# Performance work log

Measured on AMD Instinct MI355X. Metric: run time of the kernel, lower is better.

The kernel has to match this reference:

```python
import jax, jax.numpy as jnp
import numpy as np

WINDOW = 16  # window_size from init_kwargs


def sigmoid_cutoff(x):
    # max(min(1.2*sigmoid(x) - 0.1, 1), 0)
    return jnp.clip(1.2 * jax.nn.sigmoid(x) - 0.1, 0.0, 1.0)


def setup_inputs() -> dict:
    key = jax.random.key(0)
    k1, k2, k3 = jax.random.split(key, 3)
    B, S, H = 8, 2048, 1024
    x = jax.random.normal(k1, (B, S, H), dtype=jnp.float32)
    # Dense kernels (glorot-ish scale), x_layer has no bias, y_layer has bias
    Wx = jax.random.normal(k2, (H, H), dtype=jnp.float32) * (1.0 / np.sqrt(H))
    Wy = jax.random.normal(k3, (H, 2 * H), dtype=jnp.float32) * (1.0 / np.sqrt(H))
    by = jnp.zeros((2 * H,), dtype=jnp.float32)
    return {"x": x, "Wx": Wx, "Wy": Wy, "by": by}


def reference(x, Wx, Wy, by):
    B, S, H = x.shape
    # left-pad sequence with window_size-1 zeros, then project once (x_layer)
    xp = jnp.pad(x, ((0, 0), (WINDOW - 1, 0), (0, 0)))
    proj = jnp.einsum('bsh,hd->bsd', xp, Wx)  # [B, S+W-1, H]

    def step(state, i):
        # inputs[:, i:S+i] in the original loop
        inp = jax.lax.dynamic_slice_in_dim(proj, i, S, axis=1)  # [B,S,H]
        ns = jnp.einsum('bsh,hd->bsd', state, Wy) + by          # [B,S,2H]
        # reshape [B,S,2,H]: channel 0 = candidate, channel 1 = gate
        cand, gate_logits = jnp.split(ns, 2, axis=-1)
        gate = sigmoid_cutoff(gate_logits)
        new_state = jax.nn.relu(gate * (inp + cand) + (1.0 - gate) * state)
        return new_state, None

    state0 = jnp.zeros_like(x)
    state, _ = jax.lax.scan(step, state0, jnp.arange(WINDOW))
    return state
```

## Files before the change

### kernel.cpp

```cpp
#include <hip/hip_runtime.h>

#define H 1024
#define SEQ 2048
#define MROWS 16384
#define KD 1024
#define NT32 32
#define EPW 72

typedef _Float16 f16;
typedef _Float16 f16x8 __attribute__((ext_vector_type(8)));
typedef float f32x4 __attribute__((ext_vector_type(4)));

__device__ __forceinline__ float gate_fn(float x) {
    float s = 1.0f / (1.0f + __expf(-x));
    return fminf(fmaxf(1.2f * s - 0.1f, 0.0f), 1.0f);
}

__device__ __forceinline__ size_t frag_off(int row, int k) {
    return ((size_t)((row >> 4) * 32 + (k >> 5))) * 512
         + (size_t)((((row & 15) | (((k >> 3) & 3) << 4)) << 3) + (k & 7));
}

__device__ __forceinline__ void gload_lds16(const void* g, void* lds) {
    __builtin_amdgcn_global_load_lds(
        (const __attribute__((address_space(1))) unsigned int*)g,
        (__attribute__((address_space(3))) unsigned int*)lds, 16, 0, 0);
}

__global__ void k_f32_to_f16(const float* __restrict__ in, f16* __restrict__ out) {
    size_t i = ((size_t)blockIdx.x * blockDim.x + threadIdx.x) * 8;
    float4 v0 = *(const float4*)(in + i);
    float4 v1 = *(const float4*)(in + i + 4);
    f16x8 o;
    o[0] = (f16)v0.x; o[1] = (f16)v0.y; o[2] = (f16)v0.z; o[3] = (f16)v0.w;
    o[4] = (f16)v1.x; o[5] = (f16)v1.y; o[6] = (f16)v1.z; o[7] = (f16)v1.w;
    *(f16x8*)(out + i) = o;
}

__global__ void k_transpose_f16(const float* __restrict__ Wsrc, f16* __restrict__ WT,
                                int K, int N) {
    __shared__ float tile[32][33];
    int n0 = blockIdx.x * 32, k0 = blockIdx.y * 32;
    for (int i = threadIdx.y; i < 32; i += 8)
        tile[i][threadIdx.x] = Wsrc[(size_t)(k0 + i) * N + n0 + threadIdx.x];
    __syncthreads();
    for (int i = threadIdx.y; i < 32; i += 8)
        WT[(size_t)(n0 + i) * K + k0 + threadIdx.x] = (f16)tile[threadIdx.x][i];
}

__global__ __launch_bounds__(256) void k_proj_gemm(const f16* __restrict__ A,
                                                   const f16* __restrict__ BT,
                                                   f16* __restrict__ P16) {
    __shared__ alignas(16) f16 Alds[128 * 32];
    __shared__ alignas(16) f16 Blds[128 * 32];
    const int tid = threadIdx.x;
    const int lane = tid & 63, wid = tid >> 6;
    const int l15 = lane & 15, l4 = lane >> 4;
    const int bm = blockIdx.x, bn = blockIdx.y;

    const f16* gA[2]; const f16* gB[2];
    char* ldsA[2]; char* ldsB[2];
#pragma unroll
    for (int it = 0; it < 2; ++it) {
        int c = it * 4 + wid;
        int row = c * 16 + (lane >> 2);
        int kch = (lane & 3) ^ ((row >> 1) & 3);
        gA[it] = A + (size_t)(bm * 128 + row) * KD + kch * 8;
        gB[it] = BT + (size_t)(bn * 128 + row) * KD + kch * 8;
        ldsA[it] = (char*)Alds + c * 1024;
        ldsB[it] = (char*)Blds + c * 1024;
    }

    int offA[2], offB[8];
#pragma unroll
    for (int m = 0; m < 2; ++m) {
        int row = wid * 32 + m * 16 + l15;
        offA[m] = row * 64 + ((l4 ^ ((row >> 1) & 3)) << 4);
    }
#pragma unroll
    for (int n = 0; n < 8; ++n) {
        int row = n * 16 + l15;
        offB[n] = row * 64 + ((l4 ^ ((row >> 1) & 3)) << 4);
    }

    f32x4 acc[2][8] = {};

    for (int kt = 0; kt < KD / 32; ++kt) {
        __syncthreads();
#pragma unroll
        for (int it = 0; it < 2; ++it) {
            gload_lds16(gA[it], ldsA[it]);
            gload_lds16(gB[it], ldsB[it]);
            gA[it] += 32; gB[it] += 32;
        }
        __syncthreads();
        f16x8 a[2], b[8];
#pragma unroll
        for (int m = 0; m < 2; ++m) a[m] = *(const f16x8*)((const char*)Alds + offA[m]);
#pragma unroll
        for (int n = 0; n < 8; ++n) b[n] = *(const f16x8*)((const char*)Blds + offB[n]);
#pragma unroll
        for (int n = 0; n < 8; ++n)
#pragma unroll
            for (int m = 0; m < 2; ++m)
                acc[m][n] = __builtin_amdgcn_mfma_f32_16x16x32_f16(a[m], b[n], acc[m][n], 0, 0, 0);
    }

#pragma unroll
    for (int m = 0; m < 2; ++m)
#pragma unroll
        for (int n = 0; n < 8; ++n) {
            int col = bn * 128 + n * 16 + l15;
#pragma unroll
            for (int r = 0; r < 4; ++r) {
                int row = bm * 128 + wid * 32 + m * 16 + l4 * 4 + r;
                P16[(size_t)row * H + col] = (f16)acc[m][n][r];
            }
        }
}

__global__ void k_step0(const f16* __restrict__ P16, const float* __restrict__ by,
                        f16* __restrict__ S16) {
    size_t idx = ((size_t)blockIdx.x * blockDim.x + threadIdx.x) * 8;
    int row = (int)(idx >> 10);
    int d = (int)(idx & 1023);
    int s = row & (SEQ - 1);
    f16x8 p = {};
    if (s >= 15) p = *(const f16x8*)(P16 + (size_t)(row - 15) * H + d);
    float4 byc0 = *(const float4*)(by + d);
    float4 byc1 = *(const float4*)(by + d + 4);
    float4 byg0 = *(const float4*)(by + H + d);
    float4 byg1 = *(const float4*)(by + H + d + 4);
    f16x8 sv;
#pragma unroll
    for (int j = 0; j < 8; ++j) {
        float byc = (j < 4) ? ((const float*)&byc0)[j] : ((const float*)&byc1)[j - 4];
        float byg = (j < 4) ? ((const float*)&byg0)[j] : ((const float*)&byg1)[j - 4];
        float g = gate_fn(byg);
        float v = fmaxf(g * ((float)p[j] + byc), 0.f);
        sv[j] = (f16)v;
    }
    *(f16x8*)(S16 + frag_off(row, d)) = sv;
}

__global__ __launch_bounds__(512, 4) void k_step_gemm(const f16* __restrict__ A,
                                                      const f16* __restrict__ BT,
                                                      const f16* __restrict__ P16,
                                                      const float* __restrict__ by,
                                                      float* __restrict__ Out,
                                                      f16* __restrict__ Snext,
                                                      int stepi) {
    __shared__ alignas(16) char lds[73728];
    const int tid = threadIdx.x;
    const int lane = tid & 63, w = tid >> 6;
    const int l15 = lane & 15, l4 = lane >> 4;
    const int wr = w >> 1, wc = w & 1;

    const int orig = blockIdx.x;
    const int wg = (orig & 7) * 128 + (orig >> 3);
    const int bm = wg >> 4, tb = wg & 15;

    const int rB = tid >> 2;
    const int rowB = ((rB & 32) ? H : 0) + tb * 64 + ((rB >> 6) << 5) + (rB & 31);
    const int slotB = (tid & 3) ^ ((rB >> 1) & 3);
    const char* pB = (const char*)BT + ((size_t)rowB * KD + slotB * 8) * 2;

    const char* ap[4];
#pragma unroll
    for (int m = 0; m < 4; ++m) {
        int r16 = bm * 16 + wr * 4 + m;
        ap[m] = (const char*)A + ((size_t)r16 * 32) * 1024 + lane * 16;
    }

#define STAGEB(bp) do { gload_lds16(pB, (bp) + tid * 16); pB += 64; } while (0)

    const int sx = (l4 ^ ((l15 >> 1) & 3)) << 4;
    int offB[4];
#pragma unroll
    for (int n = 0; n < 4; ++n) offB[n] = (wc * 64 + n * 16 + l15) * 64 + sx;

    f32x4 acc[4][4] = {};

    char* const buf0 = lds;
    char* const buf1 = lds + 8192;
    char* cb = buf0;
    char* nx = buf1;

    STAGEB(buf0);
    __syncthreads();

#pragma unroll 1
    for (int t = 0; t < NT32; ++t) {
        f16x8 a[4];
#pragma unroll
        for (int m = 0; m < 4; ++m) { a[m] = *(const f16x8*)ap[m]; ap[m] += 1024; }
        if (t + 1 < NT32) STAGEB(nx);
        f16x8 b[4];
#pragma unroll
        for (int n = 0; n < 4; ++n) b[n] = *(const f16x8*)(cb + offB[n]);
        __builtin_amdgcn_s_setprio(1);
#pragma unroll
        for (int m = 0; m < 4; ++m)
#pragma unroll
            for (int n = 0; n < 4; ++n)
                acc[m][n] = __builtin_amdgcn_mfma_f32_16x16x32_f16(a[m], b[n], acc[m][n], 0, 0, 0);
        __builtin_amdgcn_s_setprio(0);
        __syncthreads();
        char* tmp = cb; cb = nx; nx = tmp;
    }
#undef STAGEB

    const bool last = (stepi == 15);
    f16* Cand = (f16*)lds;
    f16* Gate = (f16*)(lds + 36864);
#pragma unroll
    for (int m = 0; m < 4; ++m)
#pragma unroll
        for (int n = 0; n < 2; ++n)
#pragma unroll
            for (int r4 = 0; r4 < 4; ++r4) {
                int row = wr * 64 + m * 16 + l4 * 4 + r4;
                int cc = wc * 32 + n * 16 + l15;
                Cand[row * EPW + cc] = (f16)acc[m][n][r4];
                Gate[row * EPW + cc] = (f16)acc[m][n + 2][r4];
            }
    __syncthreads();
    {
        const int g = tid & 7;
        const int rb = tid >> 3;
        const int dl = g * 8;
        const int d = tb * 64 + dl;
        float4 byc0 = *(const float4*)(by + d);
        float4 byc1 = *(const float4*)(by + d + 4);
        float4 byg0 = *(const float4*)(by + H + d);
        float4 byg1 = *(const float4*)(by + H + d + 4);
#pragma unroll
        for (int p = 0; p < 4; ++p) {
            int row = p * 64 + rb;
            int grow = bm * 256 + row;
            int s = grow & (SEQ - 1);
            size_t fa = frag_off(grow, d);
            f16x8 c8 = *(const f16x8*)(Cand + row * EPW + dl);
            f16x8 g8 = *(const f16x8*)(Gate + row * EPW + dl);
            f16x8 p8 = {};
            if (s >= 15 - stepi)
                p8 = *(const f16x8*)(P16 + (size_t)(grow + stepi - 15) * H + d);
            f16x8 s8 = *(const f16x8*)(A + fa);
            f16x8 o8; float ov[8];
#pragma unroll
            for (int j = 0; j < 8; ++j) {
                float byc = (j < 4) ? ((const float*)&byc0)[j] : ((const float*)&byc1)[j - 4];
                float byg = (j < 4) ? ((const float*)&byg0)[j] : ((const float*)&byg1)[j - 4];
                float cand = (float)c8[j] + byc;
                float gg = gate_fn((float)g8[j] + byg);
                float v = fmaxf(gg * ((float)p8[j] + cand) + (1.f - gg) * (float)s8[j], 0.f);
                o8[j] = (f16)v; ov[j] = v;
            }
            if (!last) {
                *(f16x8*)(Snext + fa) = o8;
            } else {
                *(float4*)(Out + (size_t)grow * H + d) = make_float4(ov[0], ov[1], ov[2], ov[3]);
                *(float4*)(Out + (size_t)grow * H + d + 4) = make_float4(ov[4], ov[5], ov[6], ov[7]);
            }
        }
    }
}

extern "C" void kernel_launch(void* const* d_in, const int* in_sizes, int n_in,
                              void* d_out, int out_size, void* d_ws, size_t ws_size,
                              hipStream_t stream) {
    (void)in_sizes; (void)n_in; (void)out_size; (void)ws_size;
    const float* x  = (const float*)d_in[0];
    const float* Wx = (const float*)d_in[1];
    const float* Wy = (const float*)d_in[2];
    const float* by = (const float*)d_in[3];
    float* out = (float*)d_out;

    char* ws = (char*)d_ws;
    const size_t MB = 1024ull * 1024ull;
    f16* st16a = (f16*)(ws);
    f16* st16b = (f16*)(ws + 32 * MB);
    f16* P16   = (f16*)(ws + 64 * MB);
    f16* WxT   = (f16*)(ws + 96 * MB);
    f16* WyT   = (f16*)(ws + 98 * MB);

    hipLaunchKernelGGL(k_f32_to_f16, dim3(MROWS * H / 8 / 256), dim3(256), 0, stream, x, st16a);
    hipLaunchKernelGGL(k_transpose_f16, dim3(H / 32, H / 32), dim3(32, 8), 0, stream, Wx, WxT, H, H);
    hipLaunchKernelGGL(k_transpose_f16, dim3(2 * H / 32, H / 32), dim3(32, 8), 0, stream, Wy, WyT, H, 2 * H);
    hipLaunchKernelGGL(k_proj_gemm, dim3(MROWS / 128, H / 128), dim3(256), 0, stream, st16a, WxT, P16);
    hipLaunchKernelGGL(k_step0, dim3(MROWS * H / 8 / 256), dim3(256), 0, stream, P16, by, st16b);

    f16* bufs[2] = {st16a, st16b};
    for (int i = 1; i <= 15; ++i) {
        const f16* cur = bufs[i & 1];
        f16* nxt = bufs[(i + 1) & 1];
        hipLaunchKernelGGL(k_step_gemm, dim3(MROWS / 256 * 16), dim3(512), 0, stream,
                           cur, WyT, P16, by, out, nxt, i);
    }
}
```

Before: 1.225 ms.

## Pre-layout Wy in MFMA fragment order and load B directly from global

```diff
diff --git a/kernel.cpp b/kernel.cpp
--- a/kernel.cpp
+++ b/kernel.cpp
@@ -46,6 +46,21 @@
     __syncthreads();
     for (int i = threadIdx.y; i < 32; i += 8)
         WT[(size_t)(n0 + i) * K + k0 + threadIdx.x] = (f16)tile[threadIdx.x][i];
+}
+
+__global__ void k_transpose_fragB(const float* __restrict__ Wsrc, f16* __restrict__ WT) {
+    __shared__ float tile[32][33];
+    int n0 = blockIdx.x * 32, k0 = blockIdx.y * 32;
+    for (int i = threadIdx.y; i < 32; i += 8)
+        tile[i][threadIdx.x] = Wsrc[(size_t)(k0 + i) * (2 * H) + n0 + threadIdx.x];
+    __syncthreads();
+    int n = n0 + threadIdx.x;
+#pragma unroll
+    for (int r = 0; r < 4; ++r) {
+        int i = threadIdx.y * 4 + r;
+        int k = k0 + i;
+        WT[frag_off(n, k)] = (f16)tile[i][threadIdx.x];
+    }
 }
 
 __global__ __launch_bounds__(256) void k_proj_gemm(const f16* __restrict__ A,
@@ -144,7 +159,7 @@
 }
 
 __global__ __launch_bounds__(512, 4) void k_step_gemm(const f16* __restrict__ A,
-                                                      const f16* __restrict__ BT,
+                                                      const f16* __restrict__ WyTF,
                                                       const f16* __restrict__ P16,
                                                       const float* __restrict__ by,
                                                       float* __restrict__ Out,
@@ -160,44 +175,27 @@
     const int wg = (orig & 7) * 128 + (orig >> 3);
     const int bm = wg >> 4, tb = wg & 15;
 
-    const int rB = tid >> 2;
-    const int rowB = ((rB & 32) ? H : 0) + tb * 64 + ((rB >> 6) << 5) + (rB & 31);
-    const int slotB = (tid & 3) ^ ((rB >> 1) & 3);
-    const char* pB = (const char*)BT + ((size_t)rowB * KD + slotB * 8) * 2;
-
     const char* ap[4];
 #pragma unroll
-    for (int m = 0; m < 4; ++m) {
-        int r16 = bm * 16 + wr * 4 + m;
-        ap[m] = (const char*)A + ((size_t)r16 * 32) * 1024 + lane * 16;
-    }
-
-#define STAGEB(bp) do { gload_lds16(pB, (bp) + tid * 16); pB += 64; } while (0)
-
-    const int sx = (l4 ^ ((l15 >> 1) & 3)) << 4;
-    int offB[4];
-#pragma unroll
-    for (int n = 0; n < 4; ++n) offB[n] = (wc * 64 + n * 16 + l15) * 64 + sx;
+    for (int m = 0; m < 4; ++m)
+        ap[m] = (const char*)A + (size_t)(bm * 16 + wr * 4 + m) * 32768 + lane * 16;
+
+    const char* bp[4];
+#pragma unroll
+    for (int n = 0; n < 4; ++n) {
+        int brow16 = (n < 2) ? (tb * 4 + wc * 2 + n) : (64 + tb * 4 + wc * 2 + (n - 2));
+        bp[n] = (const char*)WyTF + (size_t)brow16 * 32768 + lane * 16;
+    }
 
     f32x4 acc[4][4] = {};
-
-    char* const buf0 = lds;
-    char* const buf1 = lds + 8192;
-    char* cb = buf0;
-    char* nx = buf1;
-
-    STAGEB(buf0);
-    __syncthreads();
 
 #pragma unroll 1
     for (int t = 0; t < NT32; ++t) {
-        f16x8 a[4];
+        f16x8 a[4], b[4];
 #pragma unroll
         for (int m = 0; m < 4; ++m) { a[m] = *(const f16x8*)ap[m]; ap[m] += 1024; }
-        if (t + 1 < NT32) STAGEB(nx);
-        f16x8 b[4];
-#pragma unroll
-        for (int n = 0; n < 4; ++n) b[n] = *(const f16x8*)(cb + offB[n]);
+#pragma unroll
+        for (int n = 0; n < 4; ++n) { b[n] = *(const f16x8*)bp[n]; bp[n] += 1024; }
         __builtin_amdgcn_s_setprio(1);
 #pragma unroll
         for (int m = 0; m < 4; ++m)
@@ -205,10 +203,7 @@
             for (int n = 0; n < 4; ++n)
                 acc[m][n] = __builtin_amdgcn_mfma_f32_16x16x32_f16(a[m], b[n], acc[m][n], 0, 0, 0);
         __builtin_amdgcn_s_setprio(0);
-        __syncthreads();
-        char* tmp = cb; cb = nx; nx = tmp;
-    }
-#undef STAGEB
+    }
 
     const bool last = (stepi == 15);
     f16* Cand = (f16*)lds;
@@ -282,11 +277,11 @@
     f16* st16b = (f16*)(ws + 32 * MB);
     f16* P16   = (f16*)(ws + 64 * MB);
     f16* WxT   = (f16*)(ws + 96 * MB);
-    f16* WyT   = (f16*)(ws + 98 * MB);
+    f16* WyTF  = (f16*)(ws + 98 * MB);
 
     hipLaunchKernelGGL(k_f32_to_f16, dim3(MROWS * H / 8 / 256), dim3(256), 0, stream, x, st16a);
     hipLaunchKernelGGL(k_transpose_f16, dim3(H / 32, H / 32), dim3(32, 8), 0, stream, Wx, WxT, H, H);
-    hipLaunchKernelGGL(k_transpose_f16, dim3(2 * H / 32, H / 32), dim3(32, 8), 0, stream, Wy, WyT, H, 2 * H);
+    hipLaunchKernelGGL(k_transpose_fragB, dim3(2 * H / 32, H / 32), dim3(32, 8), 0, stream, Wy, WyTF);
     hipLaunchKernelGGL(k_proj_gemm, dim3(MROWS / 128, H / 128), dim3(256), 0, stream, st16a, WxT, P16);
     hipLaunchKernelGGL(k_step0, dim3(MROWS * H / 8 / 256), dim3(256), 0, stream, P16, by, st16b);
 
@@ -295,6 +290,6 @@
         const f16* cur = bufs[i & 1];
         f16* nxt = bufs[(i + 1) & 1];
         hipLaunchKernelGGL(k_step_gemm, dim3(MROWS / 256 * 16), dim3(512), 0, stream,
-                           cur, WyT, P16, by, out, nxt, i);
-    }
-}
+                           cur, WyTF, P16, by, out, nxt, i);
+    }
+}
```

Measured after the change: 1.370 ms. 11.8% more time.
